# Performance work log

Hardware: AMD Instinct MI355X
Metric: run time of the kernel (lower is better)

## Reference

```python
import jax, jax.numpy as jnp
import numpy as np
import math

D_MODEL = 1024
NUM_HEADS = 16
SEQ = 2048
BATCH = 4


def setup_inputs() -> dict:
    key = jax.random.key(0)
    ks = jax.random.split(key, 7)
    s = 0.02
    return {
        "x": jax.random.normal(ks[0], (BATCH, SEQ, D_MODEL), jnp.float32),
        "Wq": jax.random.normal(ks[1], (D_MODEL, D_MODEL), jnp.float32) * s,
        "bq": jax.random.normal(ks[2], (D_MODEL,), jnp.float32) * s,
        "Wkv": jax.random.normal(ks[3], (D_MODEL, 2 * D_MODEL), jnp.float32) * s,
        "bkv": jax.random.normal(ks[4], (2 * D_MODEL,), jnp.float32) * s,
        "Wo": jax.random.normal(ks[5], (D_MODEL, D_MODEL), jnp.float32) * s,
        "bo": jax.random.normal(ks[6], (D_MODEL,), jnp.float32) * s,
        "decoderMask": 1,
    }


def reference(x, Wq, bq, Wkv, bkv, Wo, bo, decoderMask):
    B, S, D = x.shape
    H = NUM_HEADS
    dh = D // H
    q_ = x @ Wq + bq              # [B,S,D]
    kv_ = x @ Wkv + bkv           # [B,S,2D] (self-attention: m is None)
    # Faithful to source: concat [q_, kv_] then reshape into heads of 3*dh,
    # which interleaves Q/KV projection columns across heads.
    qkv = jnp.concatenate([q_, kv_], axis=-1)          # [B,S,3D]
    qkv = qkv.reshape(B, S, H, 3 * dh).transpose(0, 2, 1, 3)  # [B,H,S,3dh]
    q, k, v = jnp.split(qkv, 3, axis=-1)               # each [B,H,S,dh]
    scaled = jnp.einsum("bhqd,bhkd->bhqk", q, k) / math.sqrt(dh)
    if decoderMask:
        mask = jnp.triu(jnp.full((S, S), -jnp.inf, dtype=scaled.dtype), k=1)
        scaled = scaled + mask
    attn = jax.nn.softmax(scaled, axis=-1)
    vals = jnp.einsum("bhqk,bhkd->bhqd", attn, v)      # [B,H,S,dh]
    vals = vals.transpose(0, 2, 1, 3).reshape(B, S, D)
    return vals @ Wo + bo
```

## Files before the change

### kernel.cpp

```cpp
#include <hip/hip_runtime.h>
#include <cstddef>
#include <cstdint>

#define SEQ   2048
#define BATCH 4
#define DM    1024
#define NH    16
#define DH    64
#define ROWS  (BATCH*SEQ)
#define NC3   3072
#define SM_SCALE 0.18033688f

typedef unsigned short u16;
typedef __attribute__((ext_vector_type(8))) short bf16x8;
typedef __attribute__((ext_vector_type(2))) float f32x2;
typedef __attribute__((ext_vector_type(4))) float f32x4;
typedef __attribute__((ext_vector_type(16))) float f32x16;
typedef __attribute__((ext_vector_type(4))) unsigned u32x4;
typedef __attribute__((ext_vector_type(2))) unsigned u32x2;

union V16 { f32x16 v; f32x2 p[8]; };

__device__ __forceinline__ u16 f2b(float f) {
  union { float f; unsigned u; } v; v.f = f;
  unsigned r = v.u + 0x7fffu + ((v.u >> 16) & 1u);
  return (u16)(r >> 16);
}

__device__ __forceinline__ unsigned cvt_pk_bf16(float lo, float hi) {
  unsigned r;
  asm("v_cvt_pk_bf16_f32 %0, %1, %2" : "=v"(r) : "v"(lo), "v"(hi));
  return r;
}

__device__ __forceinline__ void plswap(unsigned& a, unsigned& b) {
  auto rr = __builtin_amdgcn_permlane32_swap((int)a, (int)b, false, false);
  a = (unsigned)rr[0];
  b = (unsigned)rr[1];
}

__device__ __forceinline__ float ex2(float x) { return __builtin_amdgcn_exp2f(x); }

__device__ __forceinline__ void gld16(const void* g, void* l) {
  __builtin_amdgcn_global_load_lds((const __attribute__((address_space(1))) void*)g,
                                   (__attribute__((address_space(3))) void*)l,
                                   16, 0, 0);
}

__global__ __launch_bounds__(256) void prep_tw_kernel(
    const float* __restrict__ x, const float* __restrict__ bq,
    const float* __restrict__ bkv, u16* __restrict__ xb, float* __restrict__ bc,
    const float* __restrict__ Wq, const float* __restrict__ Wkv,
    const float* __restrict__ Wo, u16* __restrict__ Wt)
{
  __shared__ float t_[32][33];
  const int tid = threadIdx.x;
  if (blockIdx.x < 8192) {
    int i = blockIdx.x * 256 + tid;
    int idx = i * 4;
    float4 v = *(const float4*)(x + idx);
    xb[idx + 0] = f2b(v.x);
    xb[idx + 1] = f2b(v.y);
    xb[idx + 2] = f2b(v.z);
    xb[idx + 3] = f2b(v.w);
    if (i < NC3) bc[i] = (i < DM) ? bq[i] : bkv[i - DM];
  } else {
    const int bid = blockIdx.x - 8192;
    const int n0 = (bid & 127) * 32, k0 = (bid >> 7) * 32;
    const int xcol = tid & 31, yrow = tid >> 5;
    #pragma unroll
    for (int it = 0; it < 4; ++it) {
      int k = k0 + yrow + it * 8;
      int n = n0 + xcol;
      float v;
      if (n < DM)           v = Wq[k * DM + n];
      else if (n < NC3)     v = Wkv[k * (2 * DM) + (n - DM)];
      else                  v = Wo[k * DM + (n - NC3)];
      t_[yrow + it * 8][xcol] = v;
    }
    __syncthreads();
    #pragma unroll
    for (int it = 0; it < 4; ++it) {
      int n = n0 + yrow + it * 8;
      int k = k0 + xcol;
      Wt[(size_t)n * DM + k] = f2b(t_[xcol][yrow + it * 8]);
    }
  }
}

__global__ __launch_bounds__(512, 2) void gemm8_qkv(
    const u16* __restrict__ A, const u16* __restrict__ Bt,
    const float* __restrict__ bias, u16* __restrict__ C, u16* __restrict__ Vt)
{
  constexpr int K = 1024, N = NC3;
  constexpr int ASLOT = 16384;
  constexpr int HALF  = 8192;
  constexpr int BBASE = 32768;
  __shared__ alignas(16) u16 lds_[65536];

  const int tid = threadIdx.x;
  const int lane = tid & 63, wid = tid >> 6;
  const int wr2 = wid >> 2, wc4 = wid & 3;
  const int l15 = lane & 15, lhi = lane >> 4;

  const int bid = blockIdx.x;
  const int xcd = bid & 7, t = bid >> 3;
  const int row0 = (xcd * 4 + (t & 3)) * 256;
  const int col0 = (t >> 2) * 256;

  const int sr = tid >> 3;
  const int scg = ((tid & 7) ^ (sr & 7)) * 8;
  const u16* aSrc = A  + (size_t)(row0 + sr) * K + scg;
  const u16* bSrc = Bt + (size_t)(col0 + sr) * K + scg;
  const int dLin = tid * 8;

  auto stA = [&](int kt, int h) {
    u16* d = lds_ + (kt & 1) * ASLOT + h * HALF + dLin;
    const u16* s = aSrc + (size_t)(h * 128) * K + kt * 64;
    gld16(s, d);
    gld16(s + (size_t)64 * K, d + 4096);
  };
  auto stB = [&](int kt, int h) {
    u16* d = lds_ + BBASE + (kt & 1) * ASLOT + h * HALF + dLin;
    const u16* s = bSrc + (size_t)(h * 128) * K + kt * 64;
    gld16(s, d);
    gld16(s + (size_t)64 * K, d + 4096);
  };

  int csw[2];
  csw[0] = ((lhi)     ^ (l15 & 7)) * 8;
  csw[1] = ((4 + lhi) ^ (l15 & 7)) * 8;
  const int aBase = wr2 * HALF + l15 * 64;
  const int bBase = BBASE + (wc4 >> 1) * HALF + ((wc4 & 1) * 64 + l15) * 64;

  f32x4 acc[8][4];
  #pragma unroll
  for (int m = 0; m < 8; ++m)
    #pragma unroll
    for (int n = 0; n < 4; ++n) { f32x4 z = {0.f, 0.f, 0.f, 0.f}; acc[m][n] = z; }

  stA(0, 0); stA(0, 1); stB(0, 0); stB(0, 1); stB(1, 0); stB(1, 1);
  asm volatile("s_waitcnt vmcnt(4)" ::: "memory");
  __builtin_amdgcn_s_barrier();

  constexpr int KT2 = K / 128;
  for (int j = 0; j < KT2; ++j) {
    const bool last = (j == KT2 - 1);
    #pragma unroll
    for (int hk = 0; hk < 2; ++hk) {
      const int kt = 2 * j + hk;
      const int slot = (kt & 1) * ASLOT;
      bf16x8 bfr[4][2];
      #pragma unroll
      for (int ph = 0; ph < 4; ++ph) {
        const int gp = hk * 4 + ph;
        if (ph == 0) {
          #pragma unroll
          for (int n = 0; n < 4; ++n)
            #pragma unroll
            for (int kk = 0; kk < 2; ++kk)
              bfr[n][kk] = *(const bf16x8*)&lds_[bBase + slot + n * 1024 + csw[kk]];
        }
        bf16x8 af[2][2];
        #pragma unroll
        for (int mi = 0; mi < 2; ++mi)
          #pragma unroll
          for (int kk = 0; kk < 2; ++kk)
            af[mi][kk] = *(const bf16x8*)&lds_[aBase + slot + ph * 2048 + mi * 1024 + csw[kk]];
        switch (gp) {
          case 0: stA(2 * j + 1, 0); break;
          case 1: stA(2 * j + 1, 1); break;
          case 2: if (!last) stB(2 * j + 2, 0); break;
          case 3: if (!last) stB(2 * j + 2, 1); break;
          case 4: if (!last) stA(2 * j + 2, 0); break;
          case 5: if (!last) stA(2 * j + 2, 1); break;
          case 6: if (!last) stB(2 * j + 3, 0); break;
          case 7: if (!last) stB(2 * j + 3, 1); break;
        }
        __builtin_amdgcn_s_barrier();
        asm volatile("s_waitcnt lgkmcnt(0)" ::: "memory");
        __builtin_amdgcn_sched_barrier(0);
        __builtin_amdgcn_s_setprio(1);
        #pragma unroll
        for (int mi = 0; mi < 2; ++mi)
          #pragma unroll
          for (int n = 0; n < 4; ++n) {
            acc[ph * 2 + mi][n] =
                __builtin_amdgcn_mfma_f32_16x16x32_bf16(af[mi][0], bfr[n][0], acc[ph * 2 + mi][n], 0, 0, 0);
            acc[ph * 2 + mi][n] =
                __builtin_amdgcn_mfma_f32_16x16x32_bf16(af[mi][1], bfr[n][1], acc[ph * 2 + mi][n], 0, 0, 0);
          }
        __builtin_amdgcn_s_setprio(0);
        if (gp == 3) {
          if (last) { asm volatile("s_waitcnt vmcnt(0)" ::: "memory"); }
          else      { asm volatile("s_waitcnt vmcnt(4)" ::: "memory"); }
        } else if (gp == 7 && !last) {
          asm volatile("s_waitcnt vmcnt(4)" ::: "memory");
        }
        __builtin_amdgcn_s_barrier();
      }
    }
  }

  #pragma unroll
  for (int m = 0; m < 8; ++m) {
    const int row = row0 + wr2 * 128 + m * 16 + lhi * 4;
    #pragma unroll
    for (int n = 0; n < 4; ++n) {
      const int col = col0 + wc4 * 64 + n * 16 + l15;
      const float bv = bias[col];
      const int hh = col / 192;
      const int cc = col - hh * 192;
      if (cc < 128) {
        const float qs = (cc < 64) ? SM_SCALE : 1.f;
        #pragma unroll
        for (int r = 0; r < 4; ++r)
          C[(size_t)(row + r) * N + col] = f2b((acc[m][n][r] + bv) * qs);
      } else {
        u16 wv[4];
        #pragma unroll
        for (int r = 0; r < 4; ++r) wv[r] = f2b(acc[m][n][r] + bv);
        const int bb = row >> 11, jj = row & (SEQ - 1);
        u16* vt = Vt + ((size_t)(bb * NH + hh) * 64 + (cc - 128)) * SEQ + jj;
        u32x2 pv = { (unsigned)wv[0] | ((unsigned)wv[1] << 16),
                     (unsigned)wv[2] | ((unsigned)wv[3] << 16) };
        *(u32x2*)vt = pv;
      }
    }
  }
}

__global__ __launch_bounds__(256) void gemm_out(
    const u16* __restrict__ A, const u16* __restrict__ Bt,
    const float* __restrict__ bias, float* __restrict__ C, int M, int N, int K)
{
  __shared__ alignas(16) u16 lds_[3 * 8192];
  const int tid = threadIdx.x;
  const int lane = tid & 63, wid = tid >> 6;
  const int wr = (wid >> 1) * 64, wc = (wid & 1) * 64;
  const int l15 = lane & 15, lhi = lane >> 4;

  const int bid = blockIdx.x;
  const int xcd = bid & 7, t = bid >> 3;
  const int rsub = t & 7, colb = t >> 3;
  const int row0 = (xcd * 8 + rsub) * 128, col0 = colb * 128;
  const int sr = tid >> 2;
  const int scol = (((tid & 3) ^ ((sr >> 1) & 3)) * 8);

  const u16* aS0 = A  + (size_t)(row0 + sr) * K + scol;
  const u16* aS1 = A  + (size_t)(row0 + 64 + sr) * K + scol;
  const u16* bS0 = Bt + (size_t)(col0 + sr) * K + scol;
  const u16* bS1 = Bt + (size_t)(col0 + 64 + sr) * K + scol;
  const int dA = tid * 8;

  const int csw = ((lhi ^ ((l15 >> 1) & 3)) * 8);
  int aoff[4], boff[4];
  #pragma unroll
  for (int m = 0; m < 4; ++m) aoff[m] = (wr + m * 16 + l15) * 32 + csw;
  #pragma unroll
  for (int n = 0; n < 4; ++n) boff[n] = 4096 + (wc + n * 16 + l15) * 32 + csw;

  f32x4 acc[4][4];
  #pragma unroll
  for (int m = 0; m < 4; ++m)
    #pragma unroll
    for (int n = 0; n < 4; ++n) { f32x4 z = {0.f, 0.f, 0.f, 0.f}; acc[m][n] = z; }

  const int KT = K >> 5;
  auto stage = [&](int kt, u16* base) {
    const int ka = kt * 32;
    gld16(aS0 + ka, base + dA);
    gld16(aS1 + ka, base + 2048 + dA);
    gld16(bS0 + ka, base + 4096 + dA);
    gld16(bS1 + ka, base + 6144 + dA);
  };

  u16* const bufA = lds_;
  u16* const bufB = lds_ + 8192;
  u16* const bufC = lds_ + 16384;

  stage(0, bufA); stage(1, bufB);
  asm volatile("s_waitcnt vmcnt(4)" ::: "memory");
  __builtin_amdgcn_s_barrier();

  u16* rb = bufA;
  u16* sb = bufC;
  for (int kt = 0; kt < KT; ++kt) {
    bf16x8 a[4], b[4];
    #pragma unroll
    for (int m = 0; m < 4; ++m) a[m] = *(const bf16x8*)&rb[aoff[m]];
    #pragma unroll
    for (int n = 0; n < 4; ++n) b[n] = *(const bf16x8*)&rb[boff[n]];
    if (kt + 2 < KT) stage(kt + 2, sb);
    __builtin_amdgcn_s_setprio(1);
    #pragma unroll
    for (int m = 0; m < 4; ++m)
      #pragma unroll
      for (int n = 0; n < 4; ++n)
        acc[m][n] = __builtin_amdgcn_mfma_f32_16x16x32_bf16(a[m], b[n], acc[m][n], 0, 0, 0);
    __builtin_amdgcn_s_setprio(0);
    if (kt + 1 < KT) {
      if (kt + 2 < KT) { asm volatile("s_waitcnt vmcnt(4)" ::: "memory"); }
      else             { asm volatile("s_waitcnt vmcnt(0)" ::: "memory"); }
      __builtin_amdgcn_s_barrier();
    }
    rb = (rb == bufC) ? bufA : rb + 8192;
    sb = (sb == bufC) ? bufA : sb + 8192;
  }

  #pragma unroll
  for (int m = 0; m < 4; ++m)
    #pragma unroll
    for (int n = 0; n < 4; ++n) {
      const int col = col0 + wc + n * 16 + l15;
      const float bv = bias[col];
      #pragma unroll
      for (int r = 0; r < 4; ++r) {
        const int row = row0 + wr + m * 16 + lhi * 4 + r;
        C[(size_t)row * N + col] = acc[m][n][r] + bv;
      }
    }
}

__global__ __launch_bounds__(256) void attn_kernel(
    const u16* __restrict__ qkv, const u16* __restrict__ Vt, u16* __restrict__ ctx)
{
  const int bid = blockIdx.x;
  const int p   = (bid >> 3) & 7;
  const int g   = (bid & 7) + ((bid >> 6) << 3);
  const int h   = g & 15, b = g >> 4;
  const int tid = threadIdx.x;
  const int lane = tid & 63, wid = tid >> 6;
  const int l31 = lane & 31, lhi5 = lane >> 5;

  __shared__ alignas(16) u16 smem[4 * 64 * 64];

  const size_t kv_row = (size_t)(b * NH + h) * 64;
  const int sr = tid >> 3, sck = tid & 7;
  const int scks = sck ^ (sr & 7);

  const u16* kSrc0 = qkv + (size_t)(b * SEQ + sr) * NC3 + h * 192 + 64 + scks * 8;
  const u16* kSrc1 = kSrc0 + (size_t)32 * NC3;
  const u16* vSrc0 = Vt + (kv_row + sr) * SEQ + scks * 8;
  const u16* vSrc1 = vSrc0 + (size_t)32 * SEQ;
  const int dOff0 = sr * 64 + sck * 8;
  const int dOff1 = (32 + sr) * 64 + sck * 8;

  int koff[4], koff2[4];
  #pragma unroll
  for (int c = 0; c < 4; ++c) {
    koff[c]  = l31 * 64        + (((2 * c + lhi5) ^ (l31 & 7)) * 8);
    koff2[c] = (32 + l31) * 64 + (((2 * c + lhi5) ^ (l31 & 7)) * 8);
  }

  #pragma unroll 1
  for (int half = 0; half < 2; ++half) {
    const int qt = half ? (7 - p) : (8 + p);
    const int q0 = qt * 128;

    #pragma unroll
    for (int it = 0; it < 4; ++it) {
      int row = it * 32 + sr;
      gld16(qkv + (size_t)(b * SEQ + q0 + row) * NC3 + h * 192 + scks * 8,
            &smem[row * 64 + sck * 8]);
    }
    gld16(kSrc0, &smem[8192 + dOff0]);
    gld16(kSrc1, &smem[8192 + dOff1]);
    gld16(vSrc0, &smem[12288 + dOff0]);
    gld16(vSrc1, &smem[12288 + dOff1]);
    __syncthreads();

    bf16x8 qf[4];
    {
      const int qrow = wid * 32 + l31;
      #pragma unroll
      for (int c = 0; c < 4; ++c)
        qf[c] = *(const bf16x8*)&smem[qrow * 64 + (((2 * c + lhi5) ^ (qrow & 7)) * 8)];
    }
    __syncthreads();

    V16 o0, o1;
    #pragma unroll
    for (int r = 0; r < 16; ++r) { o0.v[r] = 0.f; o1.v[r] = 0.f; }
    float lrow = 0.f;

    const int nt = qt * 2 + 2;
    const int qw0 = q0 + wid * 32;
    const int qa  = qw0 + l31;
    const int dqb = qa - 4 * lhi5;

    for (int jt = 0; jt < nt; ++jt) {
      const int j0 = jt * 64;
      const u16* Kb = smem + ((jt & 1) ? 0 : 8192);
      const u16* Vb = smem + ((jt & 1) ? 4096 : 12288);

      if (jt + 1 < nt) {
        u16* Kn = smem + ((jt & 1) ? 8192 : 0);
        u16* Vn = smem + ((jt & 1) ? 12288 : 4096);
        const size_t kAdv = (size_t)(j0 + 64) * NC3;
        const int    vAdv = j0 + 64;
        gld16(kSrc0 + kAdv, &Kn[dOff0]);
        gld16(kSrc1 + kAdv, &Kn[dOff1]);
        gld16(vSrc0 + vAdv, &Vn[dOff0]);
        gld16(vSrc1 + vAdv, &Vn[dOff1]);
      }

      if (j0 <= qw0 + 31) {
        V16 s0, s1;
        #pragma unroll
        for (int r = 0; r < 16; ++r) { s0.v[r] = 0.f; s1.v[r] = 0.f; }
        __builtin_amdgcn_s_setprio(1);
        #pragma unroll
        for (int c = 0; c < 4; ++c) {
          bf16x8 kf = *(const bf16x8*)&Kb[koff[c]];
          s0.v = __builtin_amdgcn_mfma_f32_32x32x16_bf16(kf, qf[c], s0.v, 0, 0, 0);
        }
        #pragma unroll
        for (int c = 0; c < 4; ++c) {
          bf16x8 kf = *(const bf16x8*)&Kb[koff2[c]];
          s1.v = __builtin_amdgcn_mfma_f32_32x32x16_bf16(kf, qf[c], s1.v, 0, 0, 0);
        }
        __builtin_amdgcn_s_setprio(0);

        if (j0 + 63 > qw0) {
          const int dq = dqb - j0;
          #pragma unroll
          for (int r = 0; r < 16; ++r) {
            const int kvc = (r & 3) + 8 * (r >> 2);
            s0.v[r] = (kvc > dq)      ? -1e30f : s0.v[r];
            s1.v[r] = (kvc + 32 > dq) ? -1e30f : s1.v[r];
          }
        }

        f32x2 sum2 = {0.f, 0.f};
        #pragma unroll
        for (int i = 0; i < 8; ++i) {
          f32x2 e0, e1;
          e0[0] = ex2(s0.p[i][0]); e0[1] = ex2(s0.p[i][1]);
          e1[0] = ex2(s1.p[i][0]); e1[1] = ex2(s1.p[i][1]);
          s0.p[i] = e0; s1.p[i] = e1;
          sum2 += e0 + e1;
        }
        float ps = sum2[0] + sum2[1];
        {
          unsigned a = __builtin_bit_cast(unsigned, ps), bb = a;
          plswap(a, bb);
          ps = __builtin_bit_cast(float, a) + __builtin_bit_cast(float, bb);
        }
        lrow += ps;

        unsigned pk0[8], pk1[8];
        #pragma unroll
        for (int i = 0; i < 4; ++i) {
          pk0[2 * i]     = cvt_pk_bf16(s0.v[4 * i + 0], s0.v[4 * i + 1]);
          pk0[2 * i + 1] = cvt_pk_bf16(s0.v[4 * i + 2], s0.v[4 * i + 3]);
          pk1[2 * i]     = cvt_pk_bf16(s1.v[4 * i + 0], s1.v[4 * i + 1]);
          pk1[2 * i + 1] = cvt_pk_bf16(s1.v[4 * i + 2], s1.v[4 * i + 3]);
        }
        bf16x8 pf[4];
        {
          unsigned a0 = pk0[0], b0 = pk0[2]; plswap(a0, b0);
          unsigned a1 = pk0[1], b1 = pk0[3]; plswap(a1, b1);
          u32x4 w0v = {a0, a1, b0, b1}; pf[0] = __builtin_bit_cast(bf16x8, w0v);
          unsigned a2 = pk0[4], b2 = pk0[6]; plswap(a2, b2);
          unsigned a3 = pk0[5], b3 = pk0[7]; plswap(a3, b3);
          u32x4 w1v = {a2, a3, b2, b3}; pf[1] = __builtin_bit_cast(bf16x8, w1v);
          unsigned a4 = pk1[0], b4 = pk1[2]; plswap(a4, b4);
          unsigned a5 = pk1[1], b5 = pk1[3]; plswap(a5, b5);
          u32x4 w2v = {a4, a5, b4, b5}; pf[2] = __builtin_bit_cast(bf16x8, w2v);
          unsigned a6 = pk1[4], b6 = pk1[6]; plswap(a6, b6);
          unsigned a7 = pk1[5], b7 = pk1[7]; plswap(a7, b7);
          u32x4 w3v = {a6, a7, b6, b7}; pf[3] = __builtin_bit_cast(bf16x8, w3v);
        }

        __builtin_amdgcn_s_setprio(1);
        #pragma unroll
        for (int c = 0; c < 4; ++c) {
          bf16x8 vf = *(const bf16x8*)&Vb[koff[c]];
          o0.v = __builtin_amdgcn_mfma_f32_32x32x16_bf16(vf, pf[c], o0.v, 0, 0, 0);
        }
        #pragma unroll
        for (int c = 0; c < 4; ++c) {
          bf16x8 vf = *(const bf16x8*)&Vb[koff2[c]];
          o1.v = __builtin_amdgcn_mfma_f32_32x32x16_bf16(vf, pf[c], o1.v, 0, 0, 0);
        }
        __builtin_amdgcn_s_setprio(0);
      }
      __syncthreads();
    }

    const float inv = 1.f / lrow;
    u16* crow = ctx + (size_t)(b * SEQ + qa) * DM + h * DH;
    #pragma unroll
    for (int i = 0; i < 4; ++i) {
      u32x2 v0, v1;
      v0[0] = cvt_pk_bf16(o0.v[4 * i + 0] * inv, o0.v[4 * i + 1] * inv);
      v0[1] = cvt_pk_bf16(o0.v[4 * i + 2] * inv, o0.v[4 * i + 3] * inv);
      v1[0] = cvt_pk_bf16(o1.v[4 * i + 0] * inv, o1.v[4 * i + 1] * inv);
      v1[1] = cvt_pk_bf16(o1.v[4 * i + 2] * inv, o1.v[4 * i + 3] * inv);
      *(u32x2*)&crow[8 * i + 4 * lhi5]      = v0;
      *(u32x2*)&crow[32 + 8 * i + 4 * lhi5] = v1;
    }
  }
}

extern "C" void kernel_launch(void* const* d_in, const int* in_sizes, int n_in,
                              void* d_out, int out_size, void* d_ws, size_t ws_size,
                              hipStream_t stream) {
  (void)in_sizes; (void)n_in; (void)out_size; (void)ws_size;
  const float* x   = (const float*)d_in[0];
  const float* Wq  = (const float*)d_in[1];
  const float* bq  = (const float*)d_in[2];
  const float* Wkv = (const float*)d_in[3];
  const float* bkv = (const float*)d_in[4];
  const float* Wo  = (const float*)d_in[5];
  const float* bo  = (const float*)d_in[6];
  float* out = (float*)d_out;

  char* w = (char*)d_ws;
  size_t off = 0;
  auto alloc = [&](size_t bytes) { void* p = w + off; off += (bytes + 255) & ~(size_t)255; return p; };
  u16*   xb   = (u16*)alloc((size_t)ROWS * DM * 2);
  u16*   qkvb = (u16*)alloc((size_t)ROWS * NC3 * 2);
  u16*   Vt   = (u16*)alloc((size_t)BATCH * NH * DH * SEQ * 2);
  u16*   Wt   = (u16*)alloc((size_t)4096 * DM * 2);
  float* bc   = (float*)alloc((size_t)NC3 * 4);
  u16*   ctx  = xb;

  prep_tw_kernel<<<dim3(8192 + 4096), 256, 0, stream>>>(x, bq, bkv, xb, bc, Wq, Wkv, Wo, Wt);
  gemm8_qkv<<<dim3(384), 512, 0, stream>>>(xb, Wt, bc, qkvb, Vt);
  attn_kernel<<<dim3(512), 256, 0, stream>>>(qkvb, Vt, ctx);
  gemm_out<<<dim3((ROWS / 128) * (DM / 128)), 256, 0, stream>>>(ctx, Wt + (size_t)NC3 * DM, bo, out, ROWS, DM, DM);
}
```

Before: 161.6 us.

## Shrink QKV GEMM block tile to 128x256 and double the grid

The QKV projection GEMM now uses 128-row by 256-column block tiles instead of 256x256. LDS shrinks from 128KB to 96KB per block, and each wave computes a 64x64 sub-tile with a 4x4 accumulator array instead of 8x4. The grid grows from 384 to 768 blocks to fill the GPU's CUs better and ease register and LDS pressure. In exchange, each block reuses its B tile across fewer rows, so more B data is loaded from global memory and cache in total, and the load schedule and vmcnt waits had to be reworked.

```diff
diff --git a/kernel.cpp b/kernel.cpp
--- a/kernel.cpp
+++ b/kernel.cpp
@@ -93,10 +93,10 @@
     const float* __restrict__ bias, u16* __restrict__ C, u16* __restrict__ Vt)
 {
   constexpr int K = 1024, N = NC3;
-  constexpr int ASLOT = 16384;
-  constexpr int HALF  = 8192;
-  constexpr int BBASE = 32768;
-  __shared__ alignas(16) u16 lds_[65536];
+  constexpr int ASLOT = 8192;
+  constexpr int BBASE = 16384;
+  constexpr int BSLOT = 16384;
+  __shared__ alignas(16) u16 lds_[49152];
 
   const int tid = threadIdx.x;
   const int lane = tid & 63, wid = tid >> 6;
@@ -105,8 +105,8 @@
 
   const int bid = blockIdx.x;
   const int xcd = bid & 7, t = bid >> 3;
-  const int row0 = (xcd * 4 + (t & 3)) * 256;
-  const int col0 = (t >> 2) * 256;
+  const int row0 = (xcd * 8 + (t & 7)) * 128;
+  const int col0 = (t >> 3) * 256;
 
   const int sr = tid >> 3;
   const int scg = ((tid & 7) ^ (sr & 7)) * 8;
@@ -115,31 +115,29 @@
   const int dLin = tid * 8;
 
   auto stA = [&](int kt, int h) {
-    u16* d = lds_ + (kt & 1) * ASLOT + h * HALF + dLin;
-    const u16* s = aSrc + (size_t)(h * 128) * K + kt * 64;
-    gld16(s, d);
-    gld16(s + (size_t)64 * K, d + 4096);
+    gld16(aSrc + (size_t)(h * 64) * K + kt * 64,
+          lds_ + (kt & 1) * ASLOT + h * 4096 + dLin);
   };
-  auto stB = [&](int kt, int h) {
-    u16* d = lds_ + BBASE + (kt & 1) * ASLOT + h * HALF + dLin;
-    const u16* s = bSrc + (size_t)(h * 128) * K + kt * 64;
-    gld16(s, d);
-    gld16(s + (size_t)64 * K, d + 4096);
+  auto stB = [&](int kt, int q) {
+    gld16(bSrc + (size_t)(q * 64) * K + kt * 64,
+          lds_ + BBASE + (kt & 1) * BSLOT + q * 4096 + dLin);
   };
 
   int csw[2];
   csw[0] = ((lhi)     ^ (l15 & 7)) * 8;
   csw[1] = ((4 + lhi) ^ (l15 & 7)) * 8;
-  const int aBase = wr2 * HALF + l15 * 64;
-  const int bBase = BBASE + (wc4 >> 1) * HALF + ((wc4 & 1) * 64 + l15) * 64;
-
-  f32x4 acc[8][4];
-  #pragma unroll
-  for (int m = 0; m < 8; ++m)
+  const int aBase = wr2 * 64 * 64 + l15 * 64;
+  const int bBase = BBASE + (wc4 * 64 + l15) * 64;
+
+  f32x4 acc[4][4];
+  #pragma unroll
+  for (int m = 0; m < 4; ++m)
     #pragma unroll
     for (int n = 0; n < 4; ++n) { f32x4 z = {0.f, 0.f, 0.f, 0.f}; acc[m][n] = z; }
 
-  stA(0, 0); stA(0, 1); stB(0, 0); stB(0, 1); stB(1, 0); stB(1, 1);
+  stA(0, 0); stA(0, 1);
+  stB(0, 0); stB(0, 1); stB(0, 2); stB(0, 3);
+  stB(1, 0); stB(1, 1); stB(1, 2); stB(1, 3);
   asm volatile("s_waitcnt vmcnt(4)" ::: "memory");
   __builtin_amdgcn_s_barrier();
 
@@ -148,8 +146,8 @@
     const bool last = (j == KT2 - 1);
     #pragma unroll
     for (int hk = 0; hk < 2; ++hk) {
-      const int kt = 2 * j + hk;
-      const int slot = (kt & 1) * ASLOT;
+      const int aSlot = hk * ASLOT;
+      const int bSlot = hk * BSLOT;
       bf16x8 bfr[4][2];
       #pragma unroll
       for (int ph = 0; ph < 4; ++ph) {
@@ -159,37 +157,30 @@
           for (int n = 0; n < 4; ++n)
             #pragma unroll
             for (int kk = 0; kk < 2; ++kk)
-              bfr[n][kk] = *(const bf16x8*)&lds_[bBase + slot + n * 1024 + csw[kk]];
-        }
-        bf16x8 af[2][2];
-        #pragma unroll
-        for (int mi = 0; mi < 2; ++mi)
-          #pragma unroll
-          for (int kk = 0; kk < 2; ++kk)
-            af[mi][kk] = *(const bf16x8*)&lds_[aBase + slot + ph * 2048 + mi * 1024 + csw[kk]];
+              bfr[n][kk] = *(const bf16x8*)&lds_[bBase + bSlot + n * 1024 + csw[kk]];
+        }
+        bf16x8 af[2];
+        #pragma unroll
+        for (int kk = 0; kk < 2; ++kk)
+          af[kk] = *(const bf16x8*)&lds_[aBase + aSlot + ph * 1024 + csw[kk]];
         switch (gp) {
-          case 0: stA(2 * j + 1, 0); break;
-          case 1: stA(2 * j + 1, 1); break;
-          case 2: if (!last) stB(2 * j + 2, 0); break;
-          case 3: if (!last) stB(2 * j + 2, 1); break;
-          case 4: if (!last) stA(2 * j + 2, 0); break;
-          case 5: if (!last) stA(2 * j + 2, 1); break;
-          case 6: if (!last) stB(2 * j + 3, 0); break;
-          case 7: if (!last) stB(2 * j + 3, 1); break;
+          case 0: stA(2 * j + 1, 0); stA(2 * j + 1, 1); break;
+          case 1: if (!last) { stB(2 * j + 2, 0); stB(2 * j + 2, 1); } break;
+          case 2: if (!last) { stB(2 * j + 2, 2); stB(2 * j + 2, 3); } break;
+          case 4: if (!last) { stA(2 * j + 2, 0); stA(2 * j + 2, 1); } break;
+          case 5: if (!last) { stB(2 * j + 3, 0); stB(2 * j + 3, 1); } break;
+          case 6: if (!last) { stB(2 * j + 3, 2); stB(2 * j + 3, 3); } break;
+          default: break;
         }
         __builtin_amdgcn_s_barrier();
         asm volatile("s_waitcnt lgkmcnt(0)" ::: "memory");
         __builtin_amdgcn_sched_barrier(0);
         __builtin_amdgcn_s_setprio(1);
         #pragma unroll
-        for (int mi = 0; mi < 2; ++mi)
-          #pragma unroll
-          for (int n = 0; n < 4; ++n) {
-            acc[ph * 2 + mi][n] =
-                __builtin_amdgcn_mfma_f32_16x16x32_bf16(af[mi][0], bfr[n][0], acc[ph * 2 + mi][n], 0, 0, 0);
-            acc[ph * 2 + mi][n] =
-                __builtin_amdgcn_mfma_f32_16x16x32_bf16(af[mi][1], bfr[n][1], acc[ph * 2 + mi][n], 0, 0, 0);
-          }
+        for (int n = 0; n < 4; ++n) {
+          acc[ph][n] = __builtin_amdgcn_mfma_f32_16x16x32_bf16(af[0], bfr[n][0], acc[ph][n], 0, 0, 0);
+          acc[ph][n] = __builtin_amdgcn_mfma_f32_16x16x32_bf16(af[1], bfr[n][1], acc[ph][n], 0, 0, 0);
+        }
         __builtin_amdgcn_s_setprio(0);
         if (gp == 3) {
           if (last) { asm volatile("s_waitcnt vmcnt(0)" ::: "memory"); }
@@ -203,8 +194,8 @@
   }
 
   #pragma unroll
-  for (int m = 0; m < 8; ++m) {
-    const int row = row0 + wr2 * 128 + m * 16 + lhi * 4;
+  for (int m = 0; m < 4; ++m) {
+    const int row = row0 + wr2 * 64 + m * 16 + lhi * 4;
     #pragma unroll
     for (int n = 0; n < 4; ++n) {
       const int col = col0 + wc4 * 64 + n * 16 + l15;
@@ -528,7 +519,7 @@
   u16*   ctx  = xb;
 
   prep_tw_kernel<<<dim3(8192 + 4096), 256, 0, stream>>>(x, bq, bkv, xb, bc, Wq, Wkv, Wo, Wt);
-  gemm8_qkv<<<dim3(384), 512, 0, stream>>>(xb, Wt, bc, qkvb, Vt);
+  gemm8_qkv<<<dim3(768), 512, 0, stream>>>(xb, Wt, bc, qkvb, Vt);
   attn_kernel<<<dim3(512), 256, 0, stream>>>(qkvb, Vt, ctx);
   gemm_out<<<dim3((ROWS / 128) * (DM / 128)), 256, 0, stream>>>(ctx, Wt + (size_t)NC3 * DM, bo, out, ROWS, DM, DM);
 }
```

Result: no change. 164.5 us (+1.8%).

## Use per-head 256x192 QKV tiles and run both causal halves concurrently in attention

Applied to the files above, without the earlier changes.

The QKV GEMM now uses 256x192 tiles aligned to one head's 192 columns, which gives 512 blocks instead of 384 and removes the per-element head division in the epilogue. The attention kernel goes from 256 threads that handle two query tiles one after the other to 512 threads where each half handles one tile concurrently with its own LDS region. Both halves share the barriers, so they loop to the longer trip count and the shorter half idles on masked iterations. The aim is better CU fill and less serial latency in attention, at the cost of more LDS per block, fewer active columns per wave in the GEMM, and idle waves during barrier waits.

```diff
diff --git a/kernel.cpp b/kernel.cpp
--- a/kernel.cpp
+++ b/kernel.cpp
@@ -94,9 +94,9 @@
 {
   constexpr int K = 1024, N = NC3;
   constexpr int ASLOT = 16384;
-  constexpr int HALF  = 8192;
   constexpr int BBASE = 32768;
-  __shared__ alignas(16) u16 lds_[65536];
+  constexpr int BSLOT = 12288;
+  __shared__ alignas(16) u16 lds_[57344];
 
   const int tid = threadIdx.x;
   const int lane = tid & 63, wid = tid >> 6;
@@ -106,7 +106,8 @@
   const int bid = blockIdx.x;
   const int xcd = bid & 7, t = bid >> 3;
   const int row0 = (xcd * 4 + (t & 3)) * 256;
-  const int col0 = (t >> 2) * 256;
+  const int hh   = t >> 2;
+  const int col0 = hh * 192;
 
   const int sr = tid >> 3;
   const int scg = ((tid & 7) ^ (sr & 7)) * 8;
@@ -114,33 +115,31 @@
   const u16* bSrc = Bt + (size_t)(col0 + sr) * K + scg;
   const int dLin = tid * 8;
 
-  auto stA = [&](int kt, int h) {
-    u16* d = lds_ + (kt & 1) * ASLOT + h * HALF + dLin;
-    const u16* s = aSrc + (size_t)(h * 128) * K + kt * 64;
-    gld16(s, d);
-    gld16(s + (size_t)64 * K, d + 4096);
+  auto stA = [&](int kt, int u) {
+    gld16(aSrc + (size_t)(u * 64) * K + kt * 64,
+          lds_ + (kt & 1) * ASLOT + u * 4096 + dLin);
   };
-  auto stB = [&](int kt, int h) {
-    u16* d = lds_ + BBASE + (kt & 1) * ASLOT + h * HALF + dLin;
-    const u16* s = bSrc + (size_t)(h * 128) * K + kt * 64;
-    gld16(s, d);
-    gld16(s + (size_t)64 * K, d + 4096);
+  auto stB = [&](int kt, int u) {
+    gld16(bSrc + (size_t)(u * 64) * K + kt * 64,
+          lds_ + BBASE + (kt & 1) * BSLOT + u * 4096 + dLin);
   };
 
   int csw[2];
   csw[0] = ((lhi)     ^ (l15 & 7)) * 8;
   csw[1] = ((4 + lhi) ^ (l15 & 7)) * 8;
-  const int aBase = wr2 * HALF + l15 * 64;
-  const int bBase = BBASE + (wc4 >> 1) * HALF + ((wc4 & 1) * 64 + l15) * 64;
-
-  f32x4 acc[8][4];
+  const int aBase = wr2 * 8192 + l15 * 64;
+  const int bBase = BBASE + (wc4 * 48 + l15) * 64;
+
+  f32x4 acc[8][3];
   #pragma unroll
   for (int m = 0; m < 8; ++m)
     #pragma unroll
-    for (int n = 0; n < 4; ++n) { f32x4 z = {0.f, 0.f, 0.f, 0.f}; acc[m][n] = z; }
-
-  stA(0, 0); stA(0, 1); stB(0, 0); stB(0, 1); stB(1, 0); stB(1, 1);
-  asm volatile("s_waitcnt vmcnt(4)" ::: "memory");
+    for (int n = 0; n < 3; ++n) { f32x4 z = {0.f, 0.f, 0.f, 0.f}; acc[m][n] = z; }
+
+  stA(0, 0); stA(0, 1); stA(0, 2); stA(0, 3);
+  stB(0, 0); stB(0, 1); stB(0, 2);
+  stB(1, 0); stB(1, 1); stB(1, 2);
+  asm volatile("s_waitcnt vmcnt(3)" ::: "memory");
   __builtin_amdgcn_s_barrier();
 
   constexpr int KT2 = K / 128;
@@ -148,34 +147,34 @@
     const bool last = (j == KT2 - 1);
     #pragma unroll
     for (int hk = 0; hk < 2; ++hk) {
-      const int kt = 2 * j + hk;
-      const int slot = (kt & 1) * ASLOT;
-      bf16x8 bfr[4][2];
+      const int slotA = hk * ASLOT;
+      const int slotB = hk * BSLOT;
+      bf16x8 bfr[3][2];
       #pragma unroll
       for (int ph = 0; ph < 4; ++ph) {
         const int gp = hk * 4 + ph;
         if (ph == 0) {
           #pragma unroll
-          for (int n = 0; n < 4; ++n)
+          for (int n = 0; n < 3; ++n)
             #pragma unroll
             for (int kk = 0; kk < 2; ++kk)
-              bfr[n][kk] = *(const bf16x8*)&lds_[bBase + slot + n * 1024 + csw[kk]];
+              bfr[n][kk] = *(const bf16x8*)&lds_[bBase + slotB + n * 1024 + csw[kk]];
         }
         bf16x8 af[2][2];
         #pragma unroll
         for (int mi = 0; mi < 2; ++mi)
           #pragma unroll
           for (int kk = 0; kk < 2; ++kk)
-            af[mi][kk] = *(const bf16x8*)&lds_[aBase + slot + ph * 2048 + mi * 1024 + csw[kk]];
+            af[mi][kk] = *(const bf16x8*)&lds_[aBase + slotA + (ph * 2 + mi) * 1024 + csw[kk]];
         switch (gp) {
-          case 0: stA(2 * j + 1, 0); break;
-          case 1: stA(2 * j + 1, 1); break;
-          case 2: if (!last) stB(2 * j + 2, 0); break;
-          case 3: if (!last) stB(2 * j + 2, 1); break;
-          case 4: if (!last) stA(2 * j + 2, 0); break;
-          case 5: if (!last) stA(2 * j + 2, 1); break;
-          case 6: if (!last) stB(2 * j + 3, 0); break;
-          case 7: if (!last) stB(2 * j + 3, 1); break;
+          case 0: stA(2 * j + 1, 0); stA(2 * j + 1, 1); break;
+          case 1: stA(2 * j + 1, 2); stA(2 * j + 1, 3); break;
+          case 2: if (!last) { stB(2 * j + 2, 0); stB(2 * j + 2, 1); } break;
+          case 3: if (!last) { stB(2 * j + 2, 2); } break;
+          case 4: if (!last) { stA(2 * j + 2, 0); stA(2 * j + 2, 1); } break;
+          case 5: if (!last) { stA(2 * j + 2, 2); stA(2 * j + 2, 3); } break;
+          case 6: if (!last) { stB(2 * j + 3, 0); stB(2 * j + 3, 1); } break;
+          case 7: if (!last) { stB(2 * j + 3, 2); } break;
         }
         __builtin_amdgcn_s_barrier();
         asm volatile("s_waitcnt lgkmcnt(0)" ::: "memory");
@@ -184,7 +183,7 @@
         #pragma unroll
         for (int mi = 0; mi < 2; ++mi)
           #pragma unroll
-          for (int n = 0; n < 4; ++n) {
+          for (int n = 0; n < 3; ++n) {
             acc[ph * 2 + mi][n] =
                 __builtin_amdgcn_mfma_f32_16x16x32_bf16(af[mi][0], bfr[n][0], acc[ph * 2 + mi][n], 0, 0, 0);
             acc[ph * 2 + mi][n] =
@@ -193,9 +192,9 @@
         __builtin_amdgcn_s_setprio(0);
         if (gp == 3) {
           if (last) { asm volatile("s_waitcnt vmcnt(0)" ::: "memory"); }
-          else      { asm volatile("s_waitcnt vmcnt(4)" ::: "memory"); }
+          else      { asm volatile("s_waitcnt vmcnt(3)" ::: "memory"); }
         } else if (gp == 7 && !last) {
-          asm volatile("s_waitcnt vmcnt(4)" ::: "memory");
+          asm volatile("s_waitcnt vmcnt(3)" ::: "memory");
         }
         __builtin_amdgcn_s_barrier();
       }
@@ -206,11 +205,10 @@
   for (int m = 0; m < 8; ++m) {
     const int row = row0 + wr2 * 128 + m * 16 + lhi * 4;
     #pragma unroll
-    for (int n = 0; n < 4; ++n) {
-      const int col = col0 + wc4 * 64 + n * 16 + l15;
+    for (int n = 0; n < 3; ++n) {
+      const int cc  = wc4 * 48 + n * 16 + l15;
+      const int col = col0 + cc;
       const float bv = bias[col];
-      const int hh = col / 192;
-      const int cc = col - hh * 192;
       if (cc < 128) {
         const float qs = (cc < 64) ? SM_SCALE : 1.f;
         #pragma unroll
@@ -322,7 +320,7 @@
     }
 }
 
-__global__ __launch_bounds__(256) void attn_kernel(
+__global__ __launch_bounds__(512, 4) void attn_kernel(
     const u16* __restrict__ qkv, const u16* __restrict__ Vt, u16* __restrict__ ctx)
 {
   const int bid = blockIdx.x;
@@ -330,13 +328,22 @@
   const int g   = (bid & 7) + ((bid >> 6) << 3);
   const int h   = g & 15, b = g >> 4;
   const int tid = threadIdx.x;
-  const int lane = tid & 63, wid = tid >> 6;
+  const int lane = tid & 63;
+  const int hf  = tid >> 8;
+  const int wid = (tid >> 6) & 3;
   const int l31 = lane & 31, lhi5 = lane >> 5;
 
-  __shared__ alignas(16) u16 smem[4 * 64 * 64];
+  __shared__ alignas(16) u16 smem_[2 * 16384];
+  u16* const smem = smem_ + hf * 16384;
+
+  const int qt  = hf ? (7 - p) : (8 + p);
+  const int q0  = qt * 128;
+  const int ntL = qt * 2 + 2;
+  const int ntMax = (8 + p) * 2 + 2;
 
   const size_t kv_row = (size_t)(b * NH + h) * 64;
-  const int sr = tid >> 3, sck = tid & 7;
+  const int st = tid & 255;
+  const int sr = st >> 3, sck = st & 7;
   const int scks = sck ^ (sr & 7);
 
   const u16* kSrc0 = qkv + (size_t)(b * SEQ + sr) * NC3 + h * 192 + 64 + scks * 8;
@@ -353,154 +360,148 @@
     koff2[c] = (32 + l31) * 64 + (((2 * c + lhi5) ^ (l31 & 7)) * 8);
   }
 
+  #pragma unroll
+  for (int it = 0; it < 4; ++it) {
+    int row = it * 32 + sr;
+    gld16(qkv + (size_t)(b * SEQ + q0 + row) * NC3 + h * 192 + scks * 8,
+          &smem[row * 64 + sck * 8]);
+  }
+  gld16(kSrc0, &smem[8192 + dOff0]);
+  gld16(kSrc1, &smem[8192 + dOff1]);
+  gld16(vSrc0, &smem[12288 + dOff0]);
+  gld16(vSrc1, &smem[12288 + dOff1]);
+  __syncthreads();
+
+  bf16x8 qf[4];
+  {
+    const int qrow = wid * 32 + l31;
+    #pragma unroll
+    for (int c = 0; c < 4; ++c)
+      qf[c] = *(const bf16x8*)&smem[qrow * 64 + (((2 * c + lhi5) ^ (qrow & 7)) * 8)];
+  }
+  __syncthreads();
+
+  V16 o0, o1;
+  #pragma unroll
+  for (int r = 0; r < 16; ++r) { o0.v[r] = 0.f; o1.v[r] = 0.f; }
+  float lrow = 0.f;
+
+  const int qw0 = q0 + wid * 32;
+  const int qa  = qw0 + l31;
+  const int dqb = qa - 4 * lhi5;
+
   #pragma unroll 1
-  for (int half = 0; half < 2; ++half) {
-    const int qt = half ? (7 - p) : (8 + p);
-    const int q0 = qt * 128;
-
-    #pragma unroll
-    for (int it = 0; it < 4; ++it) {
-      int row = it * 32 + sr;
-      gld16(qkv + (size_t)(b * SEQ + q0 + row) * NC3 + h * 192 + scks * 8,
-            &smem[row * 64 + sck * 8]);
-    }
-    gld16(kSrc0, &smem[8192 + dOff0]);
-    gld16(kSrc1, &smem[8192 + dOff1]);
-    gld16(vSrc0, &smem[12288 + dOff0]);
-    gld16(vSrc1, &smem[12288 + dOff1]);
+  for (int jt = 0; jt < ntMax; ++jt) {
+    const int j0 = jt * 64;
+    const u16* Kb = smem + ((jt & 1) ? 0 : 8192);
+    const u16* Vb = smem + ((jt & 1) ? 4096 : 12288);
+
+    if (jt + 1 < ntL) {
+      u16* Kn = smem + ((jt & 1) ? 8192 : 0);
+      u16* Vn = smem + ((jt & 1) ? 12288 : 4096);
+      const size_t kAdv = (size_t)(j0 + 64) * NC3;
+      const int    vAdv = j0 + 64;
+      gld16(kSrc0 + kAdv, &Kn[dOff0]);
+      gld16(kSrc1 + kAdv, &Kn[dOff1]);
+      gld16(vSrc0 + vAdv, &Vn[dOff0]);
+      gld16(vSrc1 + vAdv, &Vn[dOff1]);
+    }
+
+    if (j0 <= qw0 + 31) {
+      V16 s0, s1;
+      #pragma unroll
+      for (int r = 0; r < 16; ++r) { s0.v[r] = 0.f; s1.v[r] = 0.f; }
+      __builtin_amdgcn_s_setprio(1);
+      #pragma unroll
+      for (int c = 0; c < 4; ++c) {
+        bf16x8 kf = *(const bf16x8*)&Kb[koff[c]];
+        s0.v = __builtin_amdgcn_mfma_f32_32x32x16_bf16(kf, qf[c], s0.v, 0, 0, 0);
+      }
+      #pragma unroll
+      for (int c = 0; c < 4; ++c) {
+        bf16x8 kf = *(const bf16x8*)&Kb[koff2[c]];
+        s1.v = __builtin_amdgcn_mfma_f32_32x32x16_bf16(kf, qf[c], s1.v, 0, 0, 0);
+      }
+      __builtin_amdgcn_s_setprio(0);
+
+      if (j0 + 63 > qw0) {
+        const int dq = dqb - j0;
+        #pragma unroll
+        for (int r = 0; r < 16; ++r) {
+          const int kvc = (r & 3) + 8 * (r >> 2);
+          s0.v[r] = (kvc > dq)      ? -1e30f : s0.v[r];
+          s1.v[r] = (kvc + 32 > dq) ? -1e30f : s1.v[r];
+        }
+      }
+
+      f32x2 sum2 = {0.f, 0.f};
+      #pragma unroll
+      for (int i = 0; i < 8; ++i) {
+        f32x2 e0, e1;
+        e0[0] = ex2(s0.p[i][0]); e0[1] = ex2(s0.p[i][1]);
+        e1[0] = ex2(s1.p[i][0]); e1[1] = ex2(s1.p[i][1]);
+        s0.p[i] = e0; s1.p[i] = e1;
+        sum2 += e0 + e1;
+      }
+      float ps = sum2[0] + sum2[1];
+      {
+        unsigned a = __builtin_bit_cast(unsigned, ps), bb = a;
+        plswap(a, bb);
+        ps = __builtin_bit_cast(float, a) + __builtin_bit_cast(float, bb);
+      }
+      lrow += ps;
+
+      unsigned pk0[8], pk1[8];
+      #pragma unroll
+      for (int i = 0; i < 4; ++i) {
+        pk0[2 * i]     = cvt_pk_bf16(s0.v[4 * i + 0], s0.v[4 * i + 1]);
+        pk0[2 * i + 1] = cvt_pk_bf16(s0.v[4 * i + 2], s0.v[4 * i + 3]);
+        pk1[2 * i]     = cvt_pk_bf16(s1.v[4 * i + 0], s1.v[4 * i + 1]);
+        pk1[2 * i + 1] = cvt_pk_bf16(s1.v[4 * i + 2], s1.v[4 * i + 3]);
+      }
+      bf16x8 pf[4];
+      {
+        unsigned a0 = pk0[0], b0 = pk0[2]; plswap(a0, b0);
+        unsigned a1 = pk0[1], b1 = pk0[3]; plswap(a1, b1);
+        u32x4 w0v = {a0, a1, b0, b1}; pf[0] = __builtin_bit_cast(bf16x8, w0v);
+        unsigned a2 = pk0[4], b2 = pk0[6]; plswap(a2, b2);
+        unsigned a3 = pk0[5], b3 = pk0[7]; plswap(a3, b3);
+        u32x4 w1v = {a2, a3, b2, b3}; pf[1] = __builtin_bit_cast(bf16x8, w1v);
+        unsigned a4 = pk1[0], b4 = pk1[2]; plswap(a4, b4);
+        unsigned a5 = pk1[1], b5 = pk1[3]; plswap(a5, b5);
+        u32x4 w2v = {a4, a5, b4, b5}; pf[2] = __builtin_bit_cast(bf16x8, w2v);
+        unsigned a6 = pk1[4], b6 = pk1[6]; plswap(a6, b6);
+        unsigned a7 = pk1[5], b7 = pk1[7]; plswap(a7, b7);
+        u32x4 w3v = {a6, a7, b6, b7}; pf[3] = __builtin_bit_cast(bf16x8, w3v);
+      }
+
+      __builtin_amdgcn_s_setprio(1);
+      #pragma unroll
+      for (int c = 0; c < 4; ++c) {
+        bf16x8 vf = *(const bf16x8*)&Vb[koff[c]];
+        o0.v = __builtin_amdgcn_mfma_f32_32x32x16_bf16(vf, pf[c], o0.v, 0, 0, 0);
+      }
+      #pragma unroll
+      for (int c = 0; c < 4; ++c) {
+        bf16x8 vf = *(const bf16x8*)&Vb[koff2[c]];
+        o1.v = __builtin_amdgcn_mfma_f32_32x32x16_bf16(vf, pf[c], o1.v, 0, 0, 0);
+      }
+      __builtin_amdgcn_s_setprio(0);
+    }
     __syncthreads();
-
-    bf16x8 qf[4];
-    {
-      const int qrow = wid * 32 + l31;
-      #pragma unroll
-      for (int c = 0; c < 4; ++c)
-        qf[c] = *(const bf16x8*)&smem[qrow * 64 + (((2 * c + lhi5) ^ (qrow & 7)) * 8)];
-    }
-    __syncthreads();
-
-    V16 o0, o1;
-    #pragma unroll
-    for (int r = 0; r < 16; ++r) { o0.v[r] = 0.f; o1.v[r] = 0.f; }
-    float lrow = 0.f;
-
-    const int nt = qt * 2 + 2;
-    const int qw0 = q0 + wid * 32;
-    const int qa  = qw0 + l31;
-    const int dqb = qa - 4 * lhi5;
-
-    for (int jt = 0; jt < nt; ++jt) {
-      const int j0 = jt * 64;
-      const u16* Kb = smem + ((jt & 1) ? 0 : 8192);
-      const u16* Vb = smem + ((jt & 1) ? 4096 : 12288);
-
-      if (jt + 1 < nt) {
-        u16* Kn = smem + ((jt & 1) ? 8192 : 0);
-        u16* Vn = smem + ((jt & 1) ? 12288 : 4096);
-        const size_t kAdv = (size_t)(j0 + 64) * NC3;
-        const int    vAdv = j0 + 64;
-        gld16(kSrc0 + kAdv, &Kn[dOff0]);
-        gld16(kSrc1 + kAdv, &Kn[dOff1]);
-        gld16(vSrc0 + vAdv, &Vn[dOff0]);
-        gld16(vSrc1 + vAdv, &Vn[dOff1]);
-      }
-
-      if (j0 <= qw0 + 31) {
-        V16 s0, s1;
-        #pragma unroll
-        for (int r = 0; r < 16; ++r) { s0.v[r] = 0.f; s1.v[r] = 0.f; }
-        __builtin_amdgcn_s_setprio(1);
-        #pragma unroll
-        for (int c = 0; c < 4; ++c) {
-          bf16x8 kf = *(const bf16x8*)&Kb[koff[c]];
-          s0.v = __builtin_amdgcn_mfma_f32_32x32x16_bf16(kf, qf[c], s0.v, 0, 0, 0);
-        }
-        #pragma unroll
-        for (int c = 0; c < 4; ++c) {
-          bf16x8 kf = *(const bf16x8*)&Kb[koff2[c]];
-          s1.v = __builtin_amdgcn_mfma_f32_32x32x16_bf16(kf, qf[c], s1.v, 0, 0, 0);
-        }
-        __builtin_amdgcn_s_setprio(0);
-
-        if (j0 + 63 > qw0) {
-          const int dq = dqb - j0;
-          #pragma unroll
-          for (int r = 0; r < 16; ++r) {
-            const int kvc = (r & 3) + 8 * (r >> 2);
-            s0.v[r] = (kvc > dq)      ? -1e30f : s0.v[r];
-            s1.v[r] = (kvc + 32 > dq) ? -1e30f : s1.v[r];
-          }
-        }
-
-        f32x2 sum2 = {0.f, 0.f};
-        #pragma unroll
-        for (int i = 0; i < 8; ++i) {
-          f32x2 e0, e1;
-          e0[0] = ex2(s0.p[i][0]); e0[1] = ex2(s0.p[i][1]);
-          e1[0] = ex2(s1.p[i][0]); e1[1] = ex2(s1.p[i][1]);
-          s0.p[i] = e0; s1.p[i] = e1;
-          sum2 += e0 + e1;
-        }
-        float ps = sum2[0] + sum2[1];
-        {
-          unsigned a = __builtin_bit_cast(unsigned, ps), bb = a;
-          plswap(a, bb);
-          ps = __builtin_bit_cast(float, a) + __builtin_bit_cast(float, bb);
-        }
-        lrow += ps;
-
-        unsigned pk0[8], pk1[8];
-        #pragma unroll
-        for (int i = 0; i < 4; ++i) {
-          pk0[2 * i]     = cvt_pk_bf16(s0.v[4 * i + 0], s0.v[4 * i + 1]);
-          pk0[2 * i + 1] = cvt_pk_bf16(s0.v[4 * i + 2], s0.v[4 * i + 3]);
-          pk1[2 * i]     = cvt_pk_bf16(s1.v[4 * i + 0], s1.v[4 * i + 1]);
-          pk1[2 * i + 1] = cvt_pk_bf16(s1.v[4 * i + 2], s1.v[4 * i + 3]);
-        }
-        bf16x8 pf[4];
-        {
-          unsigned a0 = pk0[0], b0 = pk0[2]; plswap(a0, b0);
-          unsigned a1 = pk0[1], b1 = pk0[3]; plswap(a1, b1);
-          u32x4 w0v = {a0, a1, b0, b1}; pf[0] = __builtin_bit_cast(bf16x8, w0v);
-          unsigned a2 = pk0[4], b2 = pk0[6]; plswap(a2, b2);
-          unsigned a3 = pk0[5], b3 = pk0[7]; plswap(a3, b3);
-          u32x4 w1v = {a2, a3, b2, b3}; pf[1] = __builtin_bit_cast(bf16x8, w1v);
-          unsigned a4 = pk1[0], b4 = pk1[2]; plswap(a4, b4);
-          unsigned a5 = pk1[1], b5 = pk1[3]; plswap(a5, b5);
-          u32x4 w2v = {a4, a5, b4, b5}; pf[2] = __builtin_bit_cast(bf16x8, w2v);
-          unsigned a6 = pk1[4], b6 = pk1[6]; plswap(a6, b6);
-          unsigned a7 = pk1[5], b7 = pk1[7]; plswap(a7, b7);
-          u32x4 w3v = {a6, a7, b6, b7}; pf[3] = __builtin_bit_cast(bf16x8, w3v);
-        }
-
-        __builtin_amdgcn_s_setprio(1);
-        #pragma unroll
-        for (int c = 0; c < 4; ++c) {
-          bf16x8 vf = *(const bf16x8*)&Vb[koff[c]];
-          o0.v = __builtin_amdgcn_mfma_f32_32x32x16_bf16(vf, pf[c], o0.v, 0, 0, 0);
-        }
-        #pragma unroll
-        for (int c = 0; c < 4; ++c) {
-          bf16x8 vf = *(const bf16x8*)&Vb[koff2[c]];
-          o1.v = __builtin_amdgcn_mfma_f32_32x32x16_bf16(vf, pf[c], o1.v, 0, 0, 0);
-        }
-        __builtin_amdgcn_s_setprio(0);
-      }
-      __syncthreads();
-    }
-
-    const float inv = 1.f / lrow;
-    u16* crow = ctx + (size_t)(b * SEQ + qa) * DM + h * DH;
-    #pragma unroll
-    for (int i = 0; i < 4; ++i) {
-      u32x2 v0, v1;
-      v0[0] = cvt_pk_bf16(o0.v[4 * i + 0] * inv, o0.v[4 * i + 1] * inv);
-      v0[1] = cvt_pk_bf16(o0.v[4 * i + 2] * inv, o0.v[4 * i + 3] * inv);
-      v1[0] = cvt_pk_bf16(o1.v[4 * i + 0] * inv, o1.v[4 * i + 1] * inv);
-      v1[1] = cvt_pk_bf16(o1.v[4 * i + 2] * inv, o1.v[4 * i + 3] * inv);
-      *(u32x2*)&crow[8 * i + 4 * lhi5]      = v0;
-      *(u32x2*)&crow[32 + 8 * i + 4 * lhi5] = v1;
-    }
+  }
+
+  const float inv = 1.f / lrow;
+  u16* crow = ctx + (size_t)(b * SEQ + qa) * DM + h * DH;
+  #pragma unroll
+  for (int i = 0; i < 4; ++i) {
+    u32x2 v0, v1;
+    v0[0] = cvt_pk_bf16(o0.v[4 * i + 0] * inv, o0.v[4 * i + 1] * inv);
+    v0[1] = cvt_pk_bf16(o0.v[4 * i + 2] * inv, o0.v[4 * i + 3] * inv);
+    v1[0] = cvt_pk_bf16(o1.v[4 * i + 0] * inv, o1.v[4 * i + 1] * inv);
+    v1[1] = cvt_pk_bf16(o1.v[4 * i + 2] * inv, o1.v[4 * i + 3] * inv);
+    *(u32x2*)&crow[8 * i + 4 * lhi5]      = v0;
+    *(u32x2*)&crow[32 + 8 * i + 4 * lhi5] = v1;
   }
 }
 
@@ -528,7 +529,7 @@
   u16*   ctx  = xb;
 
   prep_tw_kernel<<<dim3(8192 + 4096), 256, 0, stream>>>(x, bq, bkv, xb, bc, Wq, Wkv, Wo, Wt);
-  gemm8_qkv<<<dim3(384), 512, 0, stream>>>(xb, Wt, bc, qkvb, Vt);
-  attn_kernel<<<dim3(512), 256, 0, stream>>>(qkvb, Vt, ctx);
-  gemm_out<<<dim3((ROWS / 128) * (DM / 128)), 256, 0, stream>>>(ctx, Wt + (size_t)NC3 * DM, bo, out, ROWS, DM, DM);
-}
+  gemm8_qkv<<<dim3(512), 512, 0, stream>>>(xb, Wt, bc, qkvb, Vt);
+  attn_kernel<<<dim3(512), 512, 0, stream>>>(qkvb, Vt, ctx);
+  gemm_out<<<dim3(512), 256, 0, stream>>>(ctx, Wt + (size_t)NC3 * DM, bo, out, ROWS, DM, DM);
+}
```

New measurement: 156.5 us. -3.1%, faster.
